# Kernel tuning notes

Measured on AMD Instinct MI355X. Metric: run time of the kernel, lower is better.

Reference implementation:

```python
import jax, jax.numpy as jnp
import numpy as np

N_NODES = 50000
N_EDGES = 1250000
HID = 64
N_LAYERS = 3
N_GRAPHS = 64
EPS = 1e-5


def setup_inputs() -> dict:
    key = jax.random.key(0)
    ks = jax.random.split(key, 12)
    x = jnp.arange(N_NODES, dtype=jnp.int64) if jax.config.jax_enable_x64 else jnp.arange(N_NODES, dtype=jnp.int32)
    edge_index = jax.random.randint(ks[0], (2, N_EDGES), 0, N_NODES)
    edge_weight = jax.random.uniform(ks[1], (N_EDGES,), dtype=jnp.float32)
    batch = jnp.sort(jax.random.randint(ks[2], (N_NODES,), 0, N_GRAPHS))
    # parameters
    emb = 0.02 * jax.random.normal(ks[3], (N_NODES, HID), dtype=jnp.float32)
    def xavier(k, shape):
        fan_in, fan_out = shape[-2], shape[-1]
        lim = np.sqrt(6.0 / (fan_in + fan_out))
        return jax.random.uniform(k, shape, jnp.float32, -lim, lim)
    convW = xavier(ks[4], (N_LAYERS, HID, HID))
    convB = jnp.zeros((N_LAYERS, HID), jnp.float32)
    lnG = jnp.ones((N_LAYERS, HID), jnp.float32)
    lnB = jnp.zeros((N_LAYERS, HID), jnp.float32)
    W1 = xavier(ks[5], (2 * HID, HID))
    b1 = jnp.zeros((HID,), jnp.float32)
    W2 = xavier(ks[6], (HID, 1))
    b2 = jnp.zeros((1,), jnp.float32)
    return {"x": x, "edge_index": edge_index, "edge_weight": edge_weight, "batch": batch,
            "emb": emb, "convW": convW, "convB": convB, "lnG": lnG, "lnB": lnB,
            "W1": W1, "b1": b1, "W2": W2, "b2": b2}


def _layernorm(h, g, b):
    mu = jnp.mean(h, axis=-1, keepdims=True)
    var = jnp.mean((h - mu) ** 2, axis=-1, keepdims=True)
    return (h - mu) * jax.lax.rsqrt(var + EPS) * g + b


def reference(x, edge_index, edge_weight, batch, emb, convW, convB, lnG, lnB, W1, b1, W2, b2):
    src, dst = edge_index[0], edge_index[1]
    h = emb[x]  # [N, H]
    n = h.shape[0]
    for i in range(N_LAYERS):
        m = h @ convW[i]                                   # linear transform
        msg = m[src] * edge_weight[:, None]                # gather + edge weighting
        h = jax.ops.segment_sum(msg, dst, num_segments=n)  # scatter-add aggregate
        h = h + convB[i]
        h = jax.nn.relu(_layernorm(h, lnG[i], lnB[i]))
    # pooling per graph
    counts = jax.ops.segment_sum(jnp.ones((n,), h.dtype), batch, num_segments=N_GRAPHS)
    mean_x = jax.ops.segment_sum(h, batch, num_segments=N_GRAPHS) / jnp.maximum(counts, 1.0)[:, None]
    max_x = jax.ops.segment_max(h, batch, num_segments=N_GRAPHS)
    max_x = jnp.where(counts[:, None] > 0, max_x, 0.0)
    g = jnp.concatenate([mean_x, max_x], axis=1)           # [G, 2H]
    g = jax.nn.relu(g @ W1 + b1)
    out = g @ W2 + b2
    return out.squeeze(-1)
```

## Files before the change

### kernel.cpp

```cpp
#include <hip/hip_runtime.h>

#define N_NODES 50000
#define N_EDGES 1250000
#define HID 64
#define N_LAYERS 3
#define N_GRAPHS 64
#define EPS 1e-5f

#define P_SHIFT 7
#define P_NODES 128
#define NP ((N_NODES + P_NODES - 1) / P_NODES)
#define PCAP 4096

#define LB_NODES 8

__global__ __launch_bounds__(256) void k_embed(const int* __restrict__ x,
                                               const float4* __restrict__ emb4,
                                               float4* __restrict__ h4) {
    int i = blockIdx.x * 256 + threadIdx.x;
    if (i < N_NODES * 16) {
        int row = i >> 4, q = i & 15;
        h4[i] = emb4[x[row] * 16 + q];
    }
}

__global__ __launch_bounds__(1024) void k_part(const int* __restrict__ src,
                                               const int* __restrict__ dst,
                                               const float* __restrict__ w,
                                               int* __restrict__ pcnt,
                                               int2* __restrict__ part) {
    __shared__ int hist[NP];
    __shared__ int cur[NP];
    int t = threadIdx.x;
    for (int k = t; k < NP; k += 1024) { hist[k] = 0; cur[k] = 0; }
    __syncthreads();
    int chunk = (N_EDGES + gridDim.x - 1) / gridDim.x;
    int e0 = blockIdx.x * chunk;
    int e1 = min(e0 + chunk, N_EDGES);
    for (int e = e0 + t; e < e1; e += 1024)
        atomicAdd(&hist[dst[e] >> P_SHIFT], 1);
    __syncthreads();
    for (int k = t; k < NP; k += 1024) {
        int c = hist[k];
        hist[k] = c ? atomicAdd(&pcnt[k], c) : 0;
    }
    __syncthreads();
    for (int e = e0 + t; e < e1; e += 1024) {
        int d = dst[e];
        int b = d >> P_SHIFT;
        int r = atomicAdd(&cur[b], 1);
        part[(b << 12) + hist[b] + r] =
            make_int2(((d & (P_NODES - 1)) << 16) | src[e], __float_as_int(w[e]));
    }
}

__global__ __launch_bounds__(512) void k_sort(int2* __restrict__ part,
                                              const int* __restrict__ pcnt,
                                              int* __restrict__ rowbeg,
                                              int* __restrict__ rowend,
                                              const int* __restrict__ batch,
                                              int* __restrict__ start,
                                              float* __restrict__ sums,
                                              unsigned* __restrict__ maxs) {
    __shared__ int2 sbuf[PCAP];
    __shared__ int cnt[P_NODES], base[P_NODES], cur[P_NODES];
    int p = blockIdx.x, t = threadIdx.x;
    if (t < P_NODES) cnt[t] = 0;
    __syncthreads();
    int n = pcnt[p];
    if (n > PCAP) n = PCAP;
    int2* pb = part + (p << 12);
    for (int i = t; i < n; i += 512) atomicAdd(&cnt[pb[i].x >> 16], 1);
    __syncthreads();
    if (t < P_NODES) base[t] = cnt[t];
    __syncthreads();
    for (int off = 1; off < P_NODES; off <<= 1) {
        int v = (t < P_NODES && t >= off) ? base[t - off] : 0;
        __syncthreads();
        if (t < P_NODES) base[t] += v;
        __syncthreads();
    }
    if (t < P_NODES) cur[t] = base[t] - cnt[t];
    __syncthreads();
    for (int i = t; i < n; i += 512) {
        int2 e = pb[i];
        int pos = atomicAdd(&cur[e.x >> 16], 1);
        sbuf[pos] = e;
    }
    __syncthreads();
    for (int i = t; i < n; i += 512) pb[i] = sbuf[i];
    if (t < P_NODES) {
        int node = p * P_NODES + t;
        if (node < N_NODES) {
            rowbeg[node] = (p << 12) + base[t] - cnt[t];
            rowend[node] = (p << 12) + base[t];
        }
    }
    if (p == 0) {
        if (t <= N_GRAPHS) {
            int lo = 0, hi = N_NODES;
            while (lo < hi) {
                int mid = (lo + hi) >> 1;
                if (batch[mid] < t) lo = mid + 1; else hi = mid;
            }
            start[t] = lo;
        }
        for (int k = t; k < N_GRAPHS * HID; k += 512) {
            sums[k] = 0.f;
            maxs[k] = 0u;
        }
    }
}

__global__ __launch_bounds__(512) void k_layer(const float4* __restrict__ h4,
                                               const int* __restrict__ rowbeg,
                                               const int* __restrict__ rowend,
                                               const int2* __restrict__ csr,
                                               const float* __restrict__ W,
                                               const float* __restrict__ bias,
                                               const float* __restrict__ g,
                                               const float* __restrict__ b,
                                               float* __restrict__ hout) {
    __shared__ float Wl[HID * HID];
    __shared__ float4 aggl4[LB_NODES][16];
    int tid = threadIdx.x;
    for (int k = tid; k < HID * HID; k += 512) Wl[k] = W[k];
    __syncthreads();
    int wv = tid >> 6, lane = tid & 63;
    int grp = lane >> 4, c4 = lane & 15;
    int row = blockIdx.x * LB_NODES + wv;
    int p0 = __builtin_amdgcn_readfirstlane(rowbeg[row]);
    int p1 = __builtin_amdgcn_readfirstlane(rowend[row]);
    int last = p1 - 1;
    float4 a0 = make_float4(0.f, 0.f, 0.f, 0.f);
    float4 a1 = a0, a2 = a0, a3 = a0;
    for (int p = p0; p < p1; p += 16) {
        int i0 = p + grp, i1 = i0 + 4, i2 = i0 + 8, i3 = i0 + 12;
        int2 e0 = csr[min(i0, last)];
        int2 e1 = csr[min(i1, last)];
        int2 e2 = csr[min(i2, last)];
        int2 e3 = csr[min(i3, last)];
        float w0 = (i0 <= last) ? __int_as_float(e0.y) : 0.f;
        float w1 = (i1 <= last) ? __int_as_float(e1.y) : 0.f;
        float w2 = (i2 <= last) ? __int_as_float(e2.y) : 0.f;
        float w3 = (i3 <= last) ? __int_as_float(e3.y) : 0.f;
        float4 v0 = h4[(e0.x & 0xFFFF) * 16 + c4];
        float4 v1 = h4[(e1.x & 0xFFFF) * 16 + c4];
        float4 v2 = h4[(e2.x & 0xFFFF) * 16 + c4];
        float4 v3 = h4[(e3.x & 0xFFFF) * 16 + c4];
        a0.x += v0.x * w0; a0.y += v0.y * w0; a0.z += v0.z * w0; a0.w += v0.w * w0;
        a1.x += v1.x * w1; a1.y += v1.y * w1; a1.z += v1.z * w1; a1.w += v1.w * w1;
        a2.x += v2.x * w2; a2.y += v2.y * w2; a2.z += v2.z * w2; a2.w += v2.w * w2;
        a3.x += v3.x * w3; a3.y += v3.y * w3; a3.z += v3.z * w3; a3.w += v3.w * w3;
    }
    float4 acc;
    acc.x = (a0.x + a1.x) + (a2.x + a3.x);
    acc.y = (a0.y + a1.y) + (a2.y + a3.y);
    acc.z = (a0.z + a1.z) + (a2.z + a3.z);
    acc.w = (a0.w + a1.w) + (a2.w + a3.w);
    acc.x += __shfl_xor(acc.x, 16, 64); acc.y += __shfl_xor(acc.y, 16, 64);
    acc.z += __shfl_xor(acc.z, 16, 64); acc.w += __shfl_xor(acc.w, 16, 64);
    acc.x += __shfl_xor(acc.x, 32, 64); acc.y += __shfl_xor(acc.y, 32, 64);
    acc.z += __shfl_xor(acc.z, 32, 64); acc.w += __shfl_xor(acc.w, 32, 64);
    if (grp == 0) aggl4[wv][c4] = acc;
    const float* aggl = (const float*)&aggl4[wv][0];
    int j = lane;
    float mv = 0.f;
#pragma unroll 16
    for (int k = 0; k < HID; ++k) mv += aggl[k] * Wl[k * HID + j];
    float v = mv + bias[j];
    float s = v;
#pragma unroll
    for (int off = 32; off; off >>= 1) s += __shfl_xor(s, off, 64);
    float mu = s * (1.f / 64.f);
    float d = v - mu;
    float vv = d * d;
#pragma unroll
    for (int off = 32; off; off >>= 1) vv += __shfl_xor(vv, off, 64);
    float var = vv * (1.f / 64.f);
    float y = d * rsqrtf(var + EPS) * g[j] + b[j];
    hout[row * HID + j] = fmaxf(y, 0.f);
}

#define NSLICE 16
__global__ __launch_bounds__(256) void k_pool2(const float* __restrict__ h,
                                               const int* __restrict__ start,
                                               float* __restrict__ sums,
                                               unsigned* __restrict__ maxs) {
    int gph = blockIdx.x >> 4;
    int sl  = blockIdx.x & (NSLICE - 1);
    int s = start[gph], e1 = start[gph + 1];
    int len = e1 - s;
    int chunk = (len + NSLICE - 1) / NSLICE;
    int r0 = s + sl * chunk;
    int r1 = min(r0 + chunk, e1);
    int j = threadIdx.x & 63, wv = threadIdx.x >> 6;
    float sm = 0.f, mx = 0.f;
    for (int r = r0 + wv; r < r1; r += 4) {
        float v = h[r * HID + j];
        sm += v;
        mx = fmaxf(mx, v);
    }
    atomicAdd(&sums[gph * HID + j], sm);
    atomicMax(&maxs[gph * HID + j], __float_as_uint(mx));
}

__global__ __launch_bounds__(64) void k_mlp(const float* __restrict__ sums,
                                            const unsigned* __restrict__ maxs,
                                            const int* __restrict__ start,
                                            const float* __restrict__ W1,
                                            const float* __restrict__ b1,
                                            const float* __restrict__ W2,
                                            const float* __restrict__ b2,
                                            float* __restrict__ out) {
    int gph = blockIdx.x;
    int j = threadIdx.x;
    __shared__ float gv[2 * HID];
    int cnt = start[gph + 1] - start[gph];
    float inv = 1.f / fmaxf((float)cnt, 1.f);
    gv[j] = sums[gph * HID + j] * inv;
    float mx = __uint_as_float(maxs[gph * HID + j]);
    gv[HID + j] = (cnt > 0) ? mx : 0.f;
    __syncthreads();
    float acc = b1[j];
#pragma unroll
    for (int k = 0; k < 2 * HID; ++k) acc += gv[k] * W1[k * HID + j];
    acc = fmaxf(acc, 0.f);
    float p = acc * W2[j];
#pragma unroll
    for (int off = 32; off; off >>= 1) p += __shfl_xor(p, off, 64);
    if (j == 0) out[gph] = p + b2[0];
}

extern "C" void kernel_launch(void* const* d_in, const int* in_sizes, int n_in,
                              void* d_out, int out_size, void* d_ws, size_t ws_size,
                              hipStream_t stream) {
    const int*   x     = (const int*)d_in[0];
    const int*   ei    = (const int*)d_in[1];
    const float* ew    = (const float*)d_in[2];
    const int*   batch = (const int*)d_in[3];
    const float* emb   = (const float*)d_in[4];
    const float* convW = (const float*)d_in[5];
    const float* convB = (const float*)d_in[6];
    const float* lnG   = (const float*)d_in[7];
    const float* lnB   = (const float*)d_in[8];
    const float* W1    = (const float*)d_in[9];
    const float* b1    = (const float*)d_in[10];
    const float* W2    = (const float*)d_in[11];
    const float* b2    = (const float*)d_in[12];
    float* out = (float*)d_out;

    float* hA     = (float*)d_ws;
    float* hB     = hA + (size_t)N_NODES * HID;
    int2*  part   = (int2*)(hB + (size_t)N_NODES * HID);
    int*   pcnt   = (int*)(part + (size_t)NP * PCAP);
    int*   rowbeg = pcnt + NP;
    int*   rowend = rowbeg + N_NODES;
    float* sums   = (float*)(rowend + N_NODES);
    unsigned* maxs = (unsigned*)(sums + N_GRAPHS * HID);
    int*   start  = (int*)(maxs + N_GRAPHS * HID);

    const int* src = ei;
    const int* dst = ei + N_EDGES;

    hipMemsetAsync(pcnt, 0, NP * sizeof(int), stream);
    k_part<<<256, 1024, 0, stream>>>(src, dst, ew, pcnt, part);
    k_sort<<<NP, 512, 0, stream>>>(part, pcnt, rowbeg, rowend,
                                   batch, start, sums, maxs);
    k_embed<<<(N_NODES * 16 + 255) / 256, 256, 0, stream>>>(
        x, (const float4*)emb, (float4*)hA);

    float* bufs[2] = { hA, hB };
    for (int L = 0; L < N_LAYERS; ++L) {
        k_layer<<<N_NODES / LB_NODES, 512, 0, stream>>>(
            (const float4*)bufs[L & 1], rowbeg, rowend, part,
            convW + L * HID * HID, convB + L * HID,
            lnG + L * HID, lnB + L * HID, bufs[(L + 1) & 1]);
    }
    const float* hfin = bufs[N_LAYERS & 1];

    k_pool2<<<N_GRAPHS * NSLICE, 256, 0, stream>>>(hfin, start, sums, maxs);
    k_mlp<<<N_GRAPHS, 64, 0, stream>>>(sums, maxs, start, W1, b1, W2, b2, out);
}
```

Measured before the change: 284.4 us.

## Store node features and edge weights in fp16 to halve gather traffic

Node feature buffers are now stored as fp16 and unpacked to fp32 for accumulation, so each neighbor gather reads 128 bytes instead of 256. The CSR entries are packed into a single 32-bit word (16-bit source index plus fp16 weight) written to a new array, which halves edge-list bandwidth. The gather loop is reorganised so 8 lanes cover a row and 32 edges are processed per iteration. The cost is reduced precision of features and weights, which may exceed tolerance, and the packing depends on node ids fitting in 16 bits.

```diff
diff --git a/kernel.cpp b/kernel.cpp
--- a/kernel.cpp
+++ b/kernel.cpp
@@ -1,4 +1,5 @@
 #include <hip/hip_runtime.h>
+#include <hip/hip_fp16.h>
 
 #define N_NODES 50000
 #define N_EDGES 1250000
@@ -14,13 +15,28 @@
 
 #define LB_NODES 8
 
+__device__ inline float2 up2(unsigned u) {
+    __half2 h;
+    *reinterpret_cast<unsigned*>(&h) = u;
+    return __half22float2(h);
+}
+__device__ inline unsigned pk2(float a, float b) {
+    __half2 h = __floats2half2_rn(a, b);
+    return *reinterpret_cast<unsigned*>(&h);
+}
+
 __global__ __launch_bounds__(256) void k_embed(const int* __restrict__ x,
                                                const float4* __restrict__ emb4,
-                                               float4* __restrict__ h4) {
+                                               uint4* __restrict__ h8) {
     int i = blockIdx.x * 256 + threadIdx.x;
-    if (i < N_NODES * 16) {
-        int row = i >> 4, q = i & 15;
-        h4[i] = emb4[x[row] * 16 + q];
+    if (i < N_NODES * 8) {
+        int row = i >> 3, q = i & 7;
+        float4 fa = emb4[x[row] * 16 + q * 2];
+        float4 fb = emb4[x[row] * 16 + q * 2 + 1];
+        uint4 u;
+        u.x = pk2(fa.x, fa.y); u.y = pk2(fa.z, fa.w);
+        u.z = pk2(fb.x, fb.y); u.w = pk2(fb.z, fb.w);
+        h8[i] = u;
     }
 }
 
@@ -54,8 +70,9 @@
     }
 }
 
-__global__ __launch_bounds__(512) void k_sort(int2* __restrict__ part,
+__global__ __launch_bounds__(512) void k_sort(const int2* __restrict__ part,
                                               const int* __restrict__ pcnt,
+                                              unsigned* __restrict__ csr16,
                                               int* __restrict__ rowbeg,
                                               int* __restrict__ rowend,
                                               const int* __restrict__ batch,
@@ -69,7 +86,7 @@
     __syncthreads();
     int n = pcnt[p];
     if (n > PCAP) n = PCAP;
-    int2* pb = part + (p << 12);
+    const int2* pb = part + (p << 12);
     for (int i = t; i < n; i += 512) atomicAdd(&cnt[pb[i].x >> 16], 1);
     __syncthreads();
     if (t < P_NODES) base[t] = cnt[t];
@@ -88,7 +105,11 @@
         sbuf[pos] = e;
     }
     __syncthreads();
-    for (int i = t; i < n; i += 512) pb[i] = sbuf[i];
+    for (int i = t; i < n; i += 512) {
+        int2 e = sbuf[i];
+        unsigned short wb = __half_as_ushort(__float2half_rn(__int_as_float(e.y)));
+        csr16[(p << 12) + i] = (unsigned)(e.x & 0xFFFF) | ((unsigned)wb << 16);
+    }
     if (t < P_NODES) {
         int node = p * P_NODES + t;
         if (node < N_NODES) {
@@ -112,62 +133,79 @@
     }
 }
 
-__global__ __launch_bounds__(512) void k_layer(const float4* __restrict__ h4,
+__global__ __launch_bounds__(512) void k_layer(const uint4* __restrict__ h8,
                                                const int* __restrict__ rowbeg,
                                                const int* __restrict__ rowend,
-                                               const int2* __restrict__ csr,
+                                               const unsigned* __restrict__ csr16,
                                                const float* __restrict__ W,
                                                const float* __restrict__ bias,
                                                const float* __restrict__ g,
                                                const float* __restrict__ b,
-                                               float* __restrict__ hout) {
+                                               unsigned short* __restrict__ hout) {
     __shared__ float Wl[HID * HID];
-    __shared__ float4 aggl4[LB_NODES][16];
+    __shared__ float aggl[LB_NODES][HID];
     int tid = threadIdx.x;
     for (int k = tid; k < HID * HID; k += 512) Wl[k] = W[k];
     __syncthreads();
     int wv = tid >> 6, lane = tid & 63;
-    int grp = lane >> 4, c4 = lane & 15;
+    int grp = lane >> 3, c8 = lane & 7;
     int row = blockIdx.x * LB_NODES + wv;
     int p0 = __builtin_amdgcn_readfirstlane(rowbeg[row]);
     int p1 = __builtin_amdgcn_readfirstlane(rowend[row]);
     int last = p1 - 1;
-    float4 a0 = make_float4(0.f, 0.f, 0.f, 0.f);
-    float4 a1 = a0, a2 = a0, a3 = a0;
-    for (int p = p0; p < p1; p += 16) {
-        int i0 = p + grp, i1 = i0 + 4, i2 = i0 + 8, i3 = i0 + 12;
-        int2 e0 = csr[min(i0, last)];
-        int2 e1 = csr[min(i1, last)];
-        int2 e2 = csr[min(i2, last)];
-        int2 e3 = csr[min(i3, last)];
-        float w0 = (i0 <= last) ? __int_as_float(e0.y) : 0.f;
-        float w1 = (i1 <= last) ? __int_as_float(e1.y) : 0.f;
-        float w2 = (i2 <= last) ? __int_as_float(e2.y) : 0.f;
-        float w3 = (i3 <= last) ? __int_as_float(e3.y) : 0.f;
-        float4 v0 = h4[(e0.x & 0xFFFF) * 16 + c4];
-        float4 v1 = h4[(e1.x & 0xFFFF) * 16 + c4];
-        float4 v2 = h4[(e2.x & 0xFFFF) * 16 + c4];
-        float4 v3 = h4[(e3.x & 0xFFFF) * 16 + c4];
-        a0.x += v0.x * w0; a0.y += v0.y * w0; a0.z += v0.z * w0; a0.w += v0.w * w0;
-        a1.x += v1.x * w1; a1.y += v1.y * w1; a1.z += v1.z * w1; a1.w += v1.w * w1;
-        a2.x += v2.x * w2; a2.y += v2.y * w2; a2.z += v2.z * w2; a2.w += v2.w * w2;
-        a3.x += v3.x * w3; a3.y += v3.y * w3; a3.z += v3.z * w3; a3.w += v3.w * w3;
-    }
-    float4 acc;
-    acc.x = (a0.x + a1.x) + (a2.x + a3.x);
-    acc.y = (a0.y + a1.y) + (a2.y + a3.y);
-    acc.z = (a0.z + a1.z) + (a2.z + a3.z);
-    acc.w = (a0.w + a1.w) + (a2.w + a3.w);
-    acc.x += __shfl_xor(acc.x, 16, 64); acc.y += __shfl_xor(acc.y, 16, 64);
-    acc.z += __shfl_xor(acc.z, 16, 64); acc.w += __shfl_xor(acc.w, 16, 64);
-    acc.x += __shfl_xor(acc.x, 32, 64); acc.y += __shfl_xor(acc.y, 32, 64);
-    acc.z += __shfl_xor(acc.z, 32, 64); acc.w += __shfl_xor(acc.w, 32, 64);
-    if (grp == 0) aggl4[wv][c4] = acc;
-    const float* aggl = (const float*)&aggl4[wv][0];
+    float A0[8], A1[8], A2[8], A3[8];
+#pragma unroll
+    for (int q = 0; q < 8; ++q) { A0[q] = 0.f; A1[q] = 0.f; A2[q] = 0.f; A3[q] = 0.f; }
+    for (int p = p0; p <= last; p += 32) {
+        int i0 = p + grp, i1 = i0 + 8, i2 = i0 + 16, i3 = i0 + 24;
+        unsigned e0 = csr16[min(i0, last)];
+        unsigned e1 = csr16[min(i1, last)];
+        unsigned e2 = csr16[min(i2, last)];
+        unsigned e3 = csr16[min(i3, last)];
+        float w0 = (i0 <= last) ? __half2float(__ushort_as_half((unsigned short)(e0 >> 16))) : 0.f;
+        float w1 = (i1 <= last) ? __half2float(__ushort_as_half((unsigned short)(e1 >> 16))) : 0.f;
+        float w2 = (i2 <= last) ? __half2float(__ushort_as_half((unsigned short)(e2 >> 16))) : 0.f;
+        float w3 = (i3 <= last) ? __half2float(__ushort_as_half((unsigned short)(e3 >> 16))) : 0.f;
+        uint4 v0 = h8[(e0 & 0xFFFF) * 8 + c8];
+        uint4 v1 = h8[(e1 & 0xFFFF) * 8 + c8];
+        uint4 v2 = h8[(e2 & 0xFFFF) * 8 + c8];
+        uint4 v3 = h8[(e3 & 0xFFFF) * 8 + c8];
+        float2 f;
+        f = up2(v0.x); A0[0] += f.x * w0; A0[1] += f.y * w0;
+        f = up2(v0.y); A0[2] += f.x * w0; A0[3] += f.y * w0;
+        f = up2(v0.z); A0[4] += f.x * w0; A0[5] += f.y * w0;
+        f = up2(v0.w); A0[6] += f.x * w0; A0[7] += f.y * w0;
+        f = up2(v1.x); A1[0] += f.x * w1; A1[1] += f.y * w1;
+        f = up2(v1.y); A1[2] += f.x * w1; A1[3] += f.y * w1;
+        f = up2(v1.z); A1[4] += f.x * w1; A1[5] += f.y * w1;
+        f = up2(v1.w); A1[6] += f.x * w1; A1[7] += f.y * w1;
+        f = up2(v2.x); A2[0] += f.x * w2; A2[1] += f.y * w2;
+        f = up2(v2.y); A2[2] += f.x * w2; A2[3] += f.y * w2;
+        f = up2(v2.z); A2[4] += f.x * w2; A2[5] += f.y * w2;
+        f = up2(v2.w); A2[6] += f.x * w2; A2[7] += f.y * w2;
+        f = up2(v3.x); A3[0] += f.x * w3; A3[1] += f.y * w3;
+        f = up2(v3.y); A3[2] += f.x * w3; A3[3] += f.y * w3;
+        f = up2(v3.z); A3[4] += f.x * w3; A3[5] += f.y * w3;
+        f = up2(v3.w); A3[6] += f.x * w3; A3[7] += f.y * w3;
+    }
+    float acc[8];
+#pragma unroll
+    for (int q = 0; q < 8; ++q) {
+        float s = (A0[q] + A1[q]) + (A2[q] + A3[q]);
+        s += __shfl_xor(s, 8, 64);
+        s += __shfl_xor(s, 16, 64);
+        s += __shfl_xor(s, 32, 64);
+        acc[q] = s;
+    }
+    if (grp == 0) {
+#pragma unroll
+        for (int q = 0; q < 8; ++q) aggl[wv][c8 * 8 + q] = acc[q];
+    }
+    const float* agg = &aggl[wv][0];
     int j = lane;
     float mv = 0.f;
 #pragma unroll 16
-    for (int k = 0; k < HID; ++k) mv += aggl[k] * Wl[k * HID + j];
+    for (int k = 0; k < HID; ++k) mv += agg[k] * Wl[k * HID + j];
     float v = mv + bias[j];
     float s = v;
 #pragma unroll
@@ -178,12 +216,12 @@
 #pragma unroll
     for (int off = 32; off; off >>= 1) vv += __shfl_xor(vv, off, 64);
     float var = vv * (1.f / 64.f);
-    float y = d * rsqrtf(var + EPS) * g[j] + b[j];
-    hout[row * HID + j] = fmaxf(y, 0.f);
+    float y = fmaxf(d * rsqrtf(var + EPS) * g[j] + b[j], 0.f);
+    hout[row * HID + j] = __half_as_ushort(__float2half_rn(y));
 }
 
 #define NSLICE 16
-__global__ __launch_bounds__(256) void k_pool2(const float* __restrict__ h,
+__global__ __launch_bounds__(256) void k_pool2(const unsigned short* __restrict__ h,
                                                const int* __restrict__ start,
                                                float* __restrict__ sums,
                                                unsigned* __restrict__ maxs) {
@@ -197,7 +235,7 @@
     int j = threadIdx.x & 63, wv = threadIdx.x >> 6;
     float sm = 0.f, mx = 0.f;
     for (int r = r0 + wv; r < r1; r += 4) {
-        float v = h[r * HID + j];
+        float v = __half2float(__ushort_as_half(h[r * HID + j]));
         sm += v;
         mx = fmaxf(mx, v);
     }
@@ -250,10 +288,11 @@
     const float* b2    = (const float*)d_in[12];
     float* out = (float*)d_out;
 
-    float* hA     = (float*)d_ws;
-    float* hB     = hA + (size_t)N_NODES * HID;
+    unsigned short* hA = (unsigned short*)d_ws;
+    unsigned short* hB = hA + (size_t)N_NODES * HID;
     int2*  part   = (int2*)(hB + (size_t)N_NODES * HID);
-    int*   pcnt   = (int*)(part + (size_t)NP * PCAP);
+    unsigned* csr16 = (unsigned*)(part + (size_t)NP * PCAP);
+    int*   pcnt   = (int*)(csr16 + (size_t)NP * PCAP);
     int*   rowbeg = pcnt + NP;
     int*   rowend = rowbeg + N_NODES;
     float* sums   = (float*)(rowend + N_NODES);
@@ -265,19 +304,19 @@
 
     hipMemsetAsync(pcnt, 0, NP * sizeof(int), stream);
     k_part<<<256, 1024, 0, stream>>>(src, dst, ew, pcnt, part);
-    k_sort<<<NP, 512, 0, stream>>>(part, pcnt, rowbeg, rowend,
+    k_sort<<<NP, 512, 0, stream>>>(part, pcnt, csr16, rowbeg, rowend,
                                    batch, start, sums, maxs);
-    k_embed<<<(N_NODES * 16 + 255) / 256, 256, 0, stream>>>(
-        x, (const float4*)emb, (float4*)hA);
-
-    float* bufs[2] = { hA, hB };
+    k_embed<<<(N_NODES * 8 + 255) / 256, 256, 0, stream>>>(
+        x, (const float4*)emb, (uint4*)hA);
+
+    unsigned short* bufs[2] = { hA, hB };
     for (int L = 0; L < N_LAYERS; ++L) {
         k_layer<<<N_NODES / LB_NODES, 512, 0, stream>>>(
-            (const float4*)bufs[L & 1], rowbeg, rowend, part,
+            (const uint4*)bufs[L & 1], rowbeg, rowend, csr16,
             convW + L * HID * HID, convB + L * HID,
             lnG + L * HID, lnB + L * HID, bufs[(L + 1) & 1]);
     }
-    const float* hfin = bufs[N_LAYERS & 1];
+    const unsigned short* hfin = bufs[N_LAYERS & 1];
 
     k_pool2<<<N_GRAPHS * NSLICE, 256, 0, stream>>>(hfin, start, sums, maxs);
     k_mlp<<<N_GRAPHS, 64, 0, stream>>>(sums, maxs, start, W1, b1, W2, b2, out);
```

Result: no change. 289.1 us (+1.6%).
